# Kernel optimization log

Hardware: AMD Instinct MI355X
Metric: run time of the kernel (lower is better)

The kernel has to match this reference:

```python
import jax, jax.numpy as jnp
import numpy as np

N, E, DIN, HID, HEADS = 50000, 400000, 256, 64, 4
EPS_BN = 1e-5

def setup_inputs() -> dict:
    key = jax.random.key(0)
    ks = jax.random.split(key, 12)
    inp = {}
    inp['x'] = jax.random.normal(ks[0], (N, DIN), dtype=jnp.float32)
    inp['edge_index'] = jax.random.randint(ks[1], (2, E), 0, N, dtype=jnp.int64)
    s = 1.0 / np.sqrt(DIN)
    inp['W1'] = jax.random.uniform(ks[2], (DIN, HEADS * HID), jnp.float32, -s, s)
    inp['a_src1'] = jax.random.normal(ks[3], (HEADS, HID), dtype=jnp.float32) * 0.1
    inp['a_dst1'] = jax.random.normal(ks[4], (HEADS, HID), dtype=jnp.float32) * 0.1
    inp['b1'] = jnp.zeros((HEADS * HID,), jnp.float32)
    inp['bn1_w'] = jnp.ones((HEADS * HID,), jnp.float32)
    inp['bn1_b'] = jnp.zeros((HEADS * HID,), jnp.float32)
    inp['bn1_m'] = jnp.zeros((HEADS * HID,), jnp.float32)
    inp['bn1_v'] = jnp.ones((HEADS * HID,), jnp.float32)
    s2 = 1.0 / np.sqrt(HEADS * HID)
    inp['W2'] = jax.random.uniform(ks[5], (HEADS * HID, HID), jnp.float32, -s2, s2)
    inp['a_src2'] = jax.random.normal(ks[6], (1, HID), dtype=jnp.float32) * 0.1
    inp['a_dst2'] = jax.random.normal(ks[7], (1, HID), dtype=jnp.float32) * 0.1
    inp['b2'] = jnp.zeros((HID,), jnp.float32)
    inp['bn2_w'] = jnp.ones((HID,), jnp.float32)
    inp['bn2_b'] = jnp.zeros((HID,), jnp.float32)
    inp['bn2_m'] = jnp.zeros((HID,), jnp.float32)
    inp['bn2_v'] = jnp.ones((HID,), jnp.float32)
    sr = 1.0 / np.sqrt(HID)
    inp['Wr'] = jax.random.uniform(ks[8], (HID, 1), jnp.float32, -sr, sr)
    inp['br'] = jnp.zeros((1,), jnp.float32)
    inp['Wc'] = jax.random.uniform(ks[9], (HID, 1), jnp.float32, -sr, sr)
    inp['bc'] = jnp.zeros((1,), jnp.float32)
    return inp

def gat_layer(x, src, dst, W, a_src, a_dst, bias, concat):
    # x: [N, Fin] -> h: [N, H, D]
    H, D = a_src.shape
    h = (x @ W).reshape(-1, H, D)
    alpha_s = jnp.sum(h * a_src[None], axis=-1)  # [N, H]
    alpha_d = jnp.sum(h * a_dst[None], axis=-1)
    e = jax.nn.leaky_relu(alpha_s[src] + alpha_d[dst], 0.2)  # [Et, H]
    m = jax.ops.segment_max(e, dst, num_segments=N)
    m = jnp.where(jnp.isfinite(m), m, 0.0)
    ex = jnp.exp(e - m[dst])
    denom = jax.ops.segment_sum(ex, dst, num_segments=N)
    alpha = ex / (denom[dst] + 1e-16)  # segment softmax over incoming edges
    msg = h[src] * alpha[:, :, None]  # [Et, H, D]
    out = jax.ops.segment_sum(msg, dst, num_segments=N)  # [N, H, D]
    out = out.reshape(N, H * D) if concat else out.mean(axis=1)
    return out + bias

def batchnorm(x, w, b, mean, var):
    return (x - mean) * jax.lax.rsqrt(var + EPS_BN) * w + b

def reference(x, edge_index, W1, a_src1, a_dst1, b1, bn1_w, bn1_b, bn1_m, bn1_v,
              W2, a_src2, a_dst2, b2, bn2_w, bn2_b, bn2_m, bn2_v, Wr, br, Wc, bc):
    # add self loops (PyG GATConv default)
    loops = jnp.arange(N, dtype=edge_index.dtype)
    src = jnp.concatenate([edge_index[0], loops])
    dst = jnp.concatenate([edge_index[1], loops])
    h = gat_layer(x, src, dst, W1, a_src1, a_dst1, b1, concat=True)
    h = jax.nn.elu(batchnorm(h, bn1_w, bn1_b, bn1_m, bn1_v))
    h = gat_layer(h, src, dst, W2, a_src2, a_dst2, b2, concat=False)
    h = jax.nn.elu(batchnorm(h, bn2_w, bn2_b, bn2_m, bn2_v))
    reg = h @ Wr + br
    clf = jax.nn.sigmoid(h @ Wc + bc)
    return reg, clf
```

## Files before the change

kernel.cpp:

```cpp
#include <hip/hip_runtime.h>
#include <math.h>


typedef unsigned short ushort_t;
typedef unsigned char uchar_t;
typedef __attribute__((ext_vector_type(8))) unsigned short ushort8;
typedef __attribute__((ext_vector_type(4))) unsigned short ushort4v;
typedef __attribute__((ext_vector_type(8))) short short8;
typedef __attribute__((ext_vector_type(4))) float f32x4;
typedef __attribute__((ext_vector_type(2))) float f32x2;

#define EPS_BN 1e-5f

__device__ __forceinline__ ushort_t f2bf(float f) {
  unsigned u = __float_as_uint(f);
  unsigned r = u + 0x7fffu + ((u >> 16) & 1u);
  return (ushort_t)(r >> 16);
}
__device__ __forceinline__ float bf2f(ushort_t h) {
  return __uint_as_float((unsigned)h << 16);
}
__device__ __forceinline__ uchar_t f2fp8(float f) {
  return (uchar_t)(__builtin_amdgcn_cvt_pk_fp8_f32(f, f, 0, false) & 0xff);
}
__device__ __forceinline__ float leaky02(float x) { return x >= 0.f ? x : 0.2f * x; }
__device__ __forceinline__ float elu_fast(float x) {
  return x > 0.f ? x : __expf(x) - 1.f;
}
__device__ __forceinline__ float wave_sum(float v) {
#pragma unroll
  for (int o = 1; o < 64; o <<= 1) v += __shfl_xor(v, o, 64);
  return v;
}
__device__ __forceinline__ int wave_incl_scan(int v, int lane) {
#pragma unroll
  for (int off = 1; off < 64; off <<= 1) {
    int t = __shfl_up(v, off, 64);
    if (lane >= off) v += t;
  }
  return v;
}

__device__ __forceinline__ void gld_lds16(const ushort_t* g, ushort_t* l) {
  __builtin_amdgcn_global_load_lds(
      (const __attribute__((address_space(1))) unsigned int*)g,
      (__attribute__((address_space(3))) unsigned int*)l, 16, 0, 0);
}

__global__ __launch_bounds__(256) void hist_kernel(
    const int* __restrict__ dst, int* __restrict__ counts, int E,
    const float* __restrict__ x, ushort_t* __restrict__ xb, int n8) {
  int e = blockIdx.x * blockDim.x + threadIdx.x;
  if (e < E) atomicAdd(&counts[dst[e]], 1);
  const int gsz = gridDim.x * blockDim.x;
  for (int j = e; j < n8; j += gsz) {
    float4 f0 = *(const float4*)(x + (size_t)j * 8);
    float4 f1 = *(const float4*)(x + (size_t)j * 8 + 4);
    ushort8 u;
    u[0] = f2bf(f0.x); u[1] = f2bf(f0.y); u[2] = f2bf(f0.z); u[3] = f2bf(f0.w);
    u[4] = f2bf(f1.x); u[5] = f2bf(f1.y); u[6] = f2bf(f1.z); u[7] = f2bf(f1.w);
    *(ushort8*)(xb + (size_t)j * 8) = u;
  }
}

__global__ __launch_bounds__(256) void scan_chunks_kernel(
    const int* __restrict__ counts, int* __restrict__ offsets, int* __restrict__ partials,
    int N, int E, int* __restrict__ csr_src,
    const float* __restrict__ W1, const float* __restrict__ W2,
    ushort_t* __restrict__ W1t, ushort_t* __restrict__ W2t,
    const float* __restrict__ b1, const float* __restrict__ bn1w,
    const float* __restrict__ bn1b, const float* __restrict__ bn1m,
    const float* __restrict__ bn1v,
    const float* __restrict__ b2, const float* __restrict__ bn2w,
    const float* __restrict__ bn2b, const float* __restrict__ bn2m,
    const float* __restrict__ bn2v,
    float* __restrict__ S1, float* __restrict__ T1,
    float* __restrict__ S2, float* __restrict__ T2) {
  __shared__ int ws[4];
  const int tid = threadIdx.x, lane = tid & 63, wv = tid >> 6;
  const int i = blockIdx.x * 256 + tid;
  const int gsz = gridDim.x * 256;
  int v = (i < N) ? counts[i] : 0;
  int incl = wave_incl_scan(v, lane);
  if (lane == 63) ws[wv] = incl;
  __syncthreads();
  int wbase = 0;
  for (int k = 0; k < wv; ++k) wbase += ws[k];
  if (i < N) offsets[i] = wbase + incl - v;
  if (tid == 255) partials[blockIdx.x] = wbase + incl;

  for (int j = i; j < 256 * 256; j += gsz) {
    int k = j >> 8, n2 = j & 255;
    W1t[n2 * 256 + k] = f2bf(W1[j]);
  }
  for (int j = i; j < 256 * 64; j += gsz) {
    int k = j >> 6, n2 = j & 63;
    W2t[n2 * 256 + k] = f2bf(W2[j]);
  }
  if (i < 256) {
    float s = bn1w[i] * rsqrtf(bn1v[i] + EPS_BN);
    S1[i] = s;
    T1[i] = (b1[i] - bn1m[i]) * s + bn1b[i];
  } else if (i < 320) {
    int j = i - 256;
    float s = bn2w[j] * rsqrtf(bn2v[j] + EPS_BN);
    S2[j] = s;
    T2[j] = (b2[j] - bn2m[j]) * s + bn2b[j];
  } else if (i < 384) {
    csr_src[E + i - 320] = 0;
  }
}

__global__ __launch_bounds__(256) void scatter_kernel(
    const int* __restrict__ src, const int* __restrict__ dst,
    const int* __restrict__ offsets, const int* __restrict__ partials,
    int* __restrict__ cursor, int* __restrict__ csr_src,
    int* __restrict__ offs2, int E, int N, int nb) {
  __shared__ int pp[256];
  __shared__ int ws[4];
  __shared__ int tot;
  const int tid = threadIdx.x, lane = tid & 63, wv = tid >> 6;
  int v = (tid < nb) ? partials[tid] : 0;
  int incl = wave_incl_scan(v, lane);
  if (lane == 63) ws[wv] = incl;
  __syncthreads();
  int wbase = 0;
  for (int k = 0; k < wv; ++k) wbase += ws[k];
  pp[tid] = wbase + incl - v;
  if (tid == 255) tot = wbase + incl;
  __syncthreads();

  int idx = blockIdx.x * 256 + tid;
  if (idx < E) {
    int d = dst[idx];
    int p = atomicAdd(&cursor[d], 1);
    csr_src[offsets[d] + pp[d >> 8] + p] = src[idx];
  }
  if (idx <= N) {
    offs2[idx] = (idx < N) ? offsets[idx] + pp[idx >> 8] : tot;
  }
}

template <int WM, bool CASTA, int SWZ, int OUT8>
__global__ __launch_bounds__(WM * 64) void mfma_gemm_fused(
    const void* __restrict__ Ain, const ushort_t* __restrict__ Bt,
    void* __restrict__ Cout, const float* __restrict__ avs, const float* __restrict__ avd,
    float* __restrict__ as_out, float* __restrict__ ad_out, int M, int Nt, int K, int H) {
  constexpr int BM = WM * 32;
  constexpr int NB = 4 / WM;
  __shared__ ushort_t As[BM * 32];
  __shared__ ushort_t Bs[64 * 32];
  const int t = threadIdx.x;
  const int w = t >> 6, l = t & 63;
  int m0, n0;
  if (SWZ) {
    const int Mtile = (M + BM - 1) / BM;
    const int full = (Mtile & ~7) * 4;
    int id = blockIdx.x, r, c;
    if (id < full) {
      int grp = id >> 5, wd = id & 31;
      r = grp * 8 + (wd & 7);
      c = wd >> 3;
    } else {
      int tl = id - full;
      r = (Mtile & ~7) + (tl >> 2);
      c = tl & 3;
    }
    m0 = r * BM;
    n0 = c * 64;
  } else {
    m0 = blockIdx.y * BM;
    n0 = blockIdx.x * 64;
  }
  const int head = n0 >> 6;

  f32x4 zero4 = {0.f, 0.f, 0.f, 0.f};
  f32x4 acc[2][4];
#pragma unroll
  for (int i = 0; i < 2; ++i)
#pragma unroll
    for (int j = 0; j < 4; ++j) acc[i][j] = zero4;

  const int scol = (l & 3) * 8;
  const ushort_t* Bgb[NB];
  ushort_t* Bsl[NB];
#pragma unroll
  for (int b = 0; b < NB; ++b) {
    int r = (b * WM + w) * 16 + (l >> 2);
    Bgb[b] = Bt + (size_t)(n0 + r) * K + scol;
    Bsl[b] = &Bs[(b * WM + w) * 512];
  }
  const ushort_t* Aga[2];
  ushort_t* Asl[2];
  const float* Axg = nullptr;
  ushort_t* AsWc = nullptr;
  if (CASTA) {
    int ar = t >> 1, ac = (t & 1) * 16;
    Axg = (const float*)Ain + (size_t)min(m0 + ar, M - 1) * K + ac;
    AsWc = &As[ar * 32 + ac];
  } else {
#pragma unroll
    for (int a = 0; a < 2; ++a) {
      int r = (a * WM + w) * 16 + (l >> 2);
      int gr = min(m0 + r, M - 1);
      Aga[a] = (const ushort_t*)Ain + (size_t)gr * K + scol;
      Asl[a] = &As[(a * WM + w) * 512];
    }
  }

  for (int k0 = 0; k0 < K; k0 += 32) {
    if (CASTA) {
      float4 f0 = *(const float4*)(Axg + k0);
      float4 f1 = *(const float4*)(Axg + k0 + 4);
      float4 f2 = *(const float4*)(Axg + k0 + 8);
      float4 f3 = *(const float4*)(Axg + k0 + 12);
      __syncthreads();
#pragma unroll
      for (int b = 0; b < NB; ++b) gld_lds16(Bgb[b] + k0, Bsl[b]);
      ushort8 u0, u1;
      u0[0] = f2bf(f0.x); u0[1] = f2bf(f0.y); u0[2] = f2bf(f0.z); u0[3] = f2bf(f0.w);
      u0[4] = f2bf(f1.x); u0[5] = f2bf(f1.y); u0[6] = f2bf(f1.z); u0[7] = f2bf(f1.w);
      u1[0] = f2bf(f2.x); u1[1] = f2bf(f2.y); u1[2] = f2bf(f2.z); u1[3] = f2bf(f2.w);
      u1[4] = f2bf(f3.x); u1[5] = f2bf(f3.y); u1[6] = f2bf(f3.z); u1[7] = f2bf(f3.w);
      *(ushort8*)AsWc = u0;
      *(ushort8*)(AsWc + 8) = u1;
      __syncthreads();
    } else {
      __syncthreads();
#pragma unroll
      for (int a = 0; a < 2; ++a) gld_lds16(Aga[a] + k0, Asl[a]);
#pragma unroll
      for (int b = 0; b < NB; ++b) gld_lds16(Bgb[b] + k0, Bsl[b]);
      __syncthreads();
    }
    const int kq = (l >> 4) * 8;
    short8 af[2], bfr[4];
#pragma unroll
    for (int i = 0; i < 2; ++i)
      af[i] = *(const short8*)&As[(w * 32 + i * 16 + (l & 15)) * 32 + kq];
#pragma unroll
    for (int j = 0; j < 4; ++j)
      bfr[j] = *(const short8*)&Bs[(j * 16 + (l & 15)) * 32 + kq];
#pragma unroll
    for (int i = 0; i < 2; ++i)
#pragma unroll
      for (int j = 0; j < 4; ++j)
        acc[i][j] = __builtin_amdgcn_mfma_f32_16x16x32_bf16(af[i], bfr[j], acc[i][j], 0, 0, 0);
  }

  const int rbase = m0 + w * 32 + (l >> 4) * 4;
  const int cbase = n0 + (l & 15);
#pragma unroll
  for (int i = 0; i < 2; ++i)
#pragma unroll
    for (int j = 0; j < 4; ++j)
#pragma unroll
      for (int r = 0; r < 4; ++r) {
        int row = rbase + i * 16 + r;
        if (row < M) {
          if (OUT8)
            ((uchar_t*)Cout)[(size_t)row * Nt + cbase + j * 16] = f2fp8(acc[i][j][r]);
          else
            ((ushort_t*)Cout)[(size_t)row * Nt + cbase + j * 16] = f2bf(acc[i][j][r]);
        }
      }

  float asw[4], adw[4];
#pragma unroll
  for (int j = 0; j < 4; ++j) {
    asw[j] = avs[head * 64 + (l & 15) + j * 16];
    adw[j] = avd[head * 64 + (l & 15) + j * 16];
  }
#pragma unroll
  for (int i = 0; i < 2; ++i)
#pragma unroll
    for (int r = 0; r < 4; ++r) {
      float s_ = acc[i][0][r] * asw[0] + acc[i][1][r] * asw[1] +
                 acc[i][2][r] * asw[2] + acc[i][3][r] * asw[3];
      float d_ = acc[i][0][r] * adw[0] + acc[i][1][r] * adw[1] +
                 acc[i][2][r] * adw[2] + acc[i][3][r] * adw[3];
#pragma unroll
      for (int o = 1; o < 16; o <<= 1) {
        s_ += __shfl_xor(s_, o, 64);
        d_ += __shfl_xor(d_, o, 64);
      }
      if ((l & 15) == 0) {
        int row = rbase + i * 16 + r;
        if (row < M) {
          as_out[(size_t)row * H + head] = s_;
          ad_out[(size_t)row * H + head] = d_;
        }
      }
    }
}

__global__ __launch_bounds__(256) void agg1_kernel(
    const uchar_t* __restrict__ h1, const int* __restrict__ offsets,
    const int* __restrict__ csr, const float* __restrict__ as1,
    const float* __restrict__ ad1,
    const float* __restrict__ S1, const float* __restrict__ T1,
    ushort_t* __restrict__ out, int N) {
  __shared__ float ldsW[4][64][4];
  const int wv = threadIdx.x >> 6;
  int n = blockIdx.x * 4 + wv;
  int l = threadIdx.x & 63;
  if (n >= N) return;
  const int hh = l >> 4;
  int off = offsets[n], deg = offsets[n + 1] - off;
  const int* csrp = csr + off;
  const unsigned fb = (unsigned)l << 2;
  float4 adn = *(const float4*)&ad1[n * 4];
  float ad_h = (hh & 2) ? ((hh & 1) ? adn.w : adn.z) : ((hh & 1) ? adn.y : adn.x);

  f32x2 acc0 = {0.f, 0.f}, acc1 = {0.f, 0.f};
  float den = 0.f;

  for (int base = 0; base < deg; base += 64) {
    int cnt = min(64, deg - base);
    int s = 0;
    float4 w4 = make_float4(0.f, 0.f, 0.f, 0.f);
    if (l < cnt) {
      s = csrp[base + l];
      float4 a4 = *(const float4*)&as1[s * 4];
      w4.x = __expf(leaky02(a4.x + adn.x));
      w4.y = __expf(leaky02(a4.y + adn.y));
      w4.z = __expf(leaky02(a4.z + adn.z));
      w4.w = __expf(leaky02(a4.w + adn.w));
    }
    *(float4*)&ldsW[wv][l][0] = w4;
    for (int j = 0; j < cnt; j += 8) {
#pragma unroll
      for (int i = 0; i < 8; ++i) {
        int e = j + i;
        unsigned se = (unsigned)__builtin_amdgcn_readlane(s, e);
        float we = ldsW[wv][e][hh];
        unsigned q = *(const unsigned*)(h1 + (size_t)((se << 8) + fb));
        f32x2 lo = __builtin_amdgcn_cvt_pk_f32_fp8(q, false);
        f32x2 hi = __builtin_amdgcn_cvt_pk_f32_fp8(q, true);
        f32x2 w2 = {we, we};
        acc0 = lo * w2 + acc0;
        acc1 = hi * w2 + acc1;
        den += we;
      }
    }
  }

  float4 asn = *(const float4*)&as1[n * 4];
  float as_h = (hh & 2) ? ((hh & 1) ? asn.w : asn.z) : ((hh & 1) ? asn.y : asn.x);
  float ws = __expf(leaky02(as_h + ad_h));
  {
    unsigned q = *(const unsigned*)(h1 + (size_t)(((unsigned)n << 8) + fb));
    f32x2 lo = __builtin_amdgcn_cvt_pk_f32_fp8(q, false);
    f32x2 hi = __builtin_amdgcn_cvt_pk_f32_fp8(q, true);
    f32x2 w2 = {ws, ws};
    acc0 = lo * w2 + acc0;
    acc1 = hi * w2 + acc1;
  }
  float inv = 1.f / (den + ws + 1e-16f);

  const int c0 = l * 4;
  float4 Sv = *(const float4*)&S1[c0];
  float4 Tv = *(const float4*)&T1[c0];
  float o0 = fmaf(acc0.x, inv * Sv.x, Tv.x);
  float o1 = fmaf(acc0.y, inv * Sv.y, Tv.y);
  float o2 = fmaf(acc1.x, inv * Sv.z, Tv.z);
  float o3 = fmaf(acc1.y, inv * Sv.w, Tv.w);
  ushort4v o4;
  o4[0] = f2bf(elu_fast(o0));
  o4[1] = f2bf(elu_fast(o1));
  o4[2] = f2bf(elu_fast(o2));
  o4[3] = f2bf(elu_fast(o3));
  *(ushort4v*)&out[(size_t)n * 256 + c0] = o4;
}

__global__ __launch_bounds__(256) void agg2_kernel(
    const ushort_t* __restrict__ h2, const int* __restrict__ offsets,
    const int* __restrict__ csr, const float* __restrict__ as2,
    const float* __restrict__ ad2,
    const float* __restrict__ S2, const float* __restrict__ T2,
    const float* __restrict__ Wr, const float* __restrict__ br,
    const float* __restrict__ Wc, const float* __restrict__ bc,
    float* __restrict__ out_reg, float* __restrict__ out_clf, int N) {
  __shared__ float ldsW[4][64];
  __shared__ int ldsS[4][64];
  const int wv = threadIdx.x >> 6;
  int n = blockIdx.x * 4 + wv;
  int l = threadIdx.x & 63;
  if (n >= N) return;
  const int g = l >> 4, ll = l & 15;
  int off = offsets[n], deg = offsets[n + 1] - off;
  const int* csrp = csr + off;
  const size_t hoff = (size_t)ll * 4;
  float adn = ad2[n];

  float acc[4] = {0, 0, 0, 0};
  float ds = 0.f;

  for (int base = 0; base < deg; base += 64) {
    int cnt = min(64, deg - base);
    int s = 0;
    float wv_ = 0.f;
    if (l < cnt) {
      s = csrp[base + l];
      wv_ = __expf(leaky02(as2[s] + adn));
    }
    ldsS[wv][l] = s;
    ldsW[wv][l] = wv_;
    ds += wv_;
    for (int j = 0; j < cnt; j += 16) {
      int e0 = j + g, e1 = j + 4 + g, e2 = j + 8 + g, e3 = j + 12 + g;
      int s0 = ldsS[wv][e0], s1 = ldsS[wv][e1], s2 = ldsS[wv][e2], s3 = ldsS[wv][e3];
      float w0 = ldsW[wv][e0], w1 = ldsW[wv][e1], w2 = ldsW[wv][e2], w3 = ldsW[wv][e3];
      ushort4v r0 = *(const ushort4v*)&h2[(size_t)s0 * 64 + hoff];
      ushort4v r1 = *(const ushort4v*)&h2[(size_t)s1 * 64 + hoff];
      ushort4v r2 = *(const ushort4v*)&h2[(size_t)s2 * 64 + hoff];
      ushort4v r3 = *(const ushort4v*)&h2[(size_t)s3 * 64 + hoff];
#pragma unroll
      for (int k = 0; k < 4; ++k) acc[k] = fmaf(w0, bf2f(r0[k]), acc[k]);
#pragma unroll
      for (int k = 0; k < 4; ++k) acc[k] = fmaf(w1, bf2f(r1[k]), acc[k]);
#pragma unroll
      for (int k = 0; k < 4; ++k) acc[k] = fmaf(w2, bf2f(r2[k]), acc[k]);
#pragma unroll
      for (int k = 0; k < 4; ++k) acc[k] = fmaf(w3, bf2f(r3[k]), acc[k]);
    }
  }
#pragma unroll
  for (int k = 0; k < 4; ++k) {
    acc[k] += __shfl_xor(acc[k], 16, 64);
    acc[k] += __shfl_xor(acc[k], 32, 64);
  }
  float den = wave_sum(ds);
  float ws = __expf(leaky02(as2[n] + adn));
  ushort4v hn = *(const ushort4v*)&h2[(size_t)n * 64 + hoff];
#pragma unroll
  for (int k = 0; k < 4; ++k) acc[k] = fmaf(ws, bf2f(hn[k]), acc[k]);
  float inv = 1.f / (den + ws + 1e-16f);

  int c0 = ll * 4;
  float4 Sv = *(const float4*)&S2[c0];
  float4 Tv = *(const float4*)&T2[c0];
  float4 wr = *(const float4*)&Wr[c0];
  float4 wc = *(const float4*)&Wc[c0];
  float Sf[4] = {Sv.x, Sv.y, Sv.z, Sv.w};
  float Tf[4] = {Tv.x, Tv.y, Tv.z, Tv.w};
  float wrf[4] = {wr.x, wr.y, wr.z, wr.w};
  float wcf[4] = {wc.x, wc.y, wc.z, wc.w};
  float rs = 0.f, cs = 0.f;
#pragma unroll
  for (int q = 0; q < 4; ++q) {
    float o = fmaf(acc[q], inv * Sf[q], Tf[q]);
    o = elu_fast(o);
    rs = fmaf(o, wrf[q], rs);
    cs = fmaf(o, wcf[q], cs);
  }
#pragma unroll
  for (int o = 1; o < 16; o <<= 1) {
    rs += __shfl_xor(rs, o, 64);
    cs += __shfl_xor(cs, o, 64);
  }
  if (l == 0) {
    out_reg[n] = rs + br[0];
    float z = cs + bc[0];
    out_clf[n] = 1.f / (1.f + __expf(-z));
  }
}

extern "C" void kernel_launch(void* const* d_in, const int* in_sizes, int n_in,
                              void* d_out, int out_size, void* d_ws, size_t ws_size,
                              hipStream_t stream) {
  const float* x      = (const float*)d_in[0];
  const int*   ei     = (const int*)d_in[1];
  const float* W1     = (const float*)d_in[2];
  const float* a_src1 = (const float*)d_in[3];
  const float* a_dst1 = (const float*)d_in[4];
  const float* b1     = (const float*)d_in[5];
  const float* bn1w   = (const float*)d_in[6];
  const float* bn1b   = (const float*)d_in[7];
  const float* bn1m   = (const float*)d_in[8];
  const float* bn1v   = (const float*)d_in[9];
  const float* W2     = (const float*)d_in[10];
  const float* a_src2 = (const float*)d_in[11];
  const float* a_dst2 = (const float*)d_in[12];
  const float* b2     = (const float*)d_in[13];
  const float* bn2w   = (const float*)d_in[14];
  const float* bn2b   = (const float*)d_in[15];
  const float* bn2m   = (const float*)d_in[16];
  const float* bn2v   = (const float*)d_in[17];
  const float* Wr     = (const float*)d_in[18];
  const float* br     = (const float*)d_in[19];
  const float* Wc     = (const float*)d_in[20];
  const float* bc     = (const float*)d_in[21];

  const int N = in_sizes[0] / 256;
  const int E = in_sizes[1] / 2;
  const int* srcv = ei;
  const int* dstv = ei + E;

  char* w = (char*)d_ws;
  auto alloc = [&](size_t bytes) {
    char* p = w;
    w += (bytes + 255) & ~(size_t)255;
    return p;
  };
  const int nb = (N + 255) / 256;
  const size_t nbytes_rounded = ((size_t)N * 4 + 255) & ~(size_t)255;
  int* counts    = (int*)alloc((size_t)N * 4);
  int* cursor    = (int*)alloc((size_t)N * 4);
  int* offsets   = (int*)alloc((size_t)N * 4);
  int* offs2     = (int*)alloc((size_t)(N + 1) * 4);
  int* partials  = (int*)alloc((size_t)nb * 4);
  int* csr_src   = (int*)alloc((size_t)(E + 64) * 4);
  float* as1     = (float*)alloc((size_t)N * 4 * 4);
  float* ad1     = (float*)alloc((size_t)N * 4 * 4);
  float* as2     = (float*)alloc((size_t)N * 4);
  float* ad2     = (float*)alloc((size_t)N * 4);
  float* S1      = (float*)alloc(256 * 4);
  float* T1      = (float*)alloc(256 * 4);
  float* S2      = (float*)alloc(64 * 4);
  float* T2      = (float*)alloc(64 * 4);
  ushort_t* W1t  = (ushort_t*)alloc((size_t)256 * 256 * 2);
  ushort_t* W2t  = (ushort_t*)alloc((size_t)64 * 256 * 2);
  ushort_t* xb   = (ushort_t*)alloc((size_t)N * 256 * 2);
  uchar_t* h1b   = (uchar_t*)alloc((size_t)N * 256);
  ushort_t* h1a  = (ushort_t*)alloc((size_t)N * 256 * 2);
  ushort_t* h2b  = (ushort_t*)alloc((size_t)N * 64 * 2);

  float* out_reg = (float*)d_out;

  hipMemsetAsync(counts, 0, nbytes_rounded * 2, stream);
  hist_kernel<<<(E + 255) / 256, 256, 0, stream>>>(dstv, counts, E, x, xb, N * 256 / 8);
  scan_chunks_kernel<<<nb, 256, 0, stream>>>(counts, offsets, partials, N, E, csr_src,
                                             W1, W2, W1t, W2t,
                                             b1, bn1w, bn1b, bn1m, bn1v,
                                             b2, bn2w, bn2b, bn2m, bn2v,
                                             S1, T1, S2, T2);
  {
    int items = max(E, N + 1);
    scatter_kernel<<<(items + 255) / 256, 256, 0, stream>>>(srcv, dstv, offsets, partials,
                                                            cursor, csr_src, offs2, E, N, nb);
  }

  const int nwb = (N + 3) / 4;

  const int mtiles = (N + 127) / 128;
  mfma_gemm_fused<4, false, 1, 1><<<mtiles * 4, 256, 0, stream>>>(
      xb, W1t, h1b, a_src1, a_dst1, as1, ad1, N, 256, 256, 4);
  agg1_kernel<<<nwb, 256, 0, stream>>>(h1b, offs2, csr_src, as1, ad1, S1, T1, h1a, N);

  dim3 g2(1, (N + 63) / 64);
  mfma_gemm_fused<2, false, 0, 0><<<g2, 128, 0, stream>>>(h1a, W2t, h2b, a_src2, a_dst2,
                                                          as2, ad2, N, 64, 256, 1);
  agg2_kernel<<<nwb, 256, 0, stream>>>(h2b, offs2, csr_src, as2, ad2, S2, T2,
                                       Wr, br, Wc, bc, out_reg, out_reg + N, N);
}
```

Before: 260.7 us.

## Replace K-looped GEMM with full-K LDS-resident tiles and XCD-aware block remap

Both GEMMs now use one kernel that loads the whole 64x256 A tile and 64x256 B tile into LDS in a single pass, with an XOR swizzle against bank conflicts, and then runs the MFMA loop with no further barriers. This removes the per-K-step syncthreads and the load/compute serialization of the old 32-wide K loop. The first GEMM also remaps block IDs so neighbouring tiles land on the same XCD. The cost is 64 KB of LDS per block, which limits occupancy, and a 64-row M tile instead of 128 for layer 1.

```diff
diff --git a/kernel.cpp b/kernel.cpp
--- a/kernel.cpp
+++ b/kernel.cpp
@@ -141,157 +141,106 @@
   }
 }
 
-template <int WM, bool CASTA, int SWZ, int OUT8>
-__global__ __launch_bounds__(WM * 64) void mfma_gemm_fused(
-    const void* __restrict__ Ain, const ushort_t* __restrict__ Bt,
+template <int H, int OUT8, int SWZ>
+__global__ __launch_bounds__(256) void gemm_fullk(
+    const ushort_t* __restrict__ Ain, const ushort_t* __restrict__ Bt,
     void* __restrict__ Cout, const float* __restrict__ avs, const float* __restrict__ avd,
-    float* __restrict__ as_out, float* __restrict__ ad_out, int M, int Nt, int K, int H) {
-  constexpr int BM = WM * 32;
-  constexpr int NB = 4 / WM;
-  __shared__ ushort_t As[BM * 32];
-  __shared__ ushort_t Bs[64 * 32];
+    float* __restrict__ as_out, float* __restrict__ ad_out, int M) {
+  constexpr int NT = H * 64;
+  __shared__ ushort_t As[64 * 256];
+  __shared__ ushort_t Bs[64 * 256];
   const int t = threadIdx.x;
   const int w = t >> 6, l = t & 63;
-  int m0, n0;
+
+  int id = blockIdx.x;
   if (SWZ) {
-    const int Mtile = (M + BM - 1) / BM;
-    const int full = (Mtile & ~7) * 4;
-    int id = blockIdx.x, r, c;
-    if (id < full) {
-      int grp = id >> 5, wd = id & 31;
-      r = grp * 8 + (wd & 7);
-      c = wd >> 3;
-    } else {
-      int tl = id - full;
-      r = (Mtile & ~7) + (tl >> 2);
-      c = tl & 3;
-    }
-    m0 = r * BM;
-    n0 = c * 64;
-  } else {
-    m0 = blockIdx.y * BM;
-    n0 = blockIdx.x * 64;
-  }
-  const int head = n0 >> 6;
-
-  f32x4 zero4 = {0.f, 0.f, 0.f, 0.f};
-  f32x4 acc[2][4];
-#pragma unroll
-  for (int i = 0; i < 2; ++i)
-#pragma unroll
-    for (int j = 0; j < 4; ++j) acc[i][j] = zero4;
-
-  const int scol = (l & 3) * 8;
-  const ushort_t* Bgb[NB];
-  ushort_t* Bsl[NB];
-#pragma unroll
-  for (int b = 0; b < NB; ++b) {
-    int r = (b * WM + w) * 16 + (l >> 2);
-    Bgb[b] = Bt + (size_t)(n0 + r) * K + scol;
-    Bsl[b] = &Bs[(b * WM + w) * 512];
-  }
-  const ushort_t* Aga[2];
-  ushort_t* Asl[2];
-  const float* Axg = nullptr;
-  ushort_t* AsWc = nullptr;
-  if (CASTA) {
-    int ar = t >> 1, ac = (t & 1) * 16;
-    Axg = (const float*)Ain + (size_t)min(m0 + ar, M - 1) * K + ac;
-    AsWc = &As[ar * 32 + ac];
-  } else {
-#pragma unroll
-    for (int a = 0; a < 2; ++a) {
-      int r = (a * WM + w) * 16 + (l >> 2);
-      int gr = min(m0 + r, M - 1);
-      Aga[a] = (const ushort_t*)Ain + (size_t)gr * K + scol;
-      Asl[a] = &As[(a * WM + w) * 512];
-    }
-  }
-
-  for (int k0 = 0; k0 < K; k0 += 32) {
-    if (CASTA) {
-      float4 f0 = *(const float4*)(Axg + k0);
-      float4 f1 = *(const float4*)(Axg + k0 + 4);
-      float4 f2 = *(const float4*)(Axg + k0 + 8);
-      float4 f3 = *(const float4*)(Axg + k0 + 12);
-      __syncthreads();
-#pragma unroll
-      for (int b = 0; b < NB; ++b) gld_lds16(Bgb[b] + k0, Bsl[b]);
-      ushort8 u0, u1;
-      u0[0] = f2bf(f0.x); u0[1] = f2bf(f0.y); u0[2] = f2bf(f0.z); u0[3] = f2bf(f0.w);
-      u0[4] = f2bf(f1.x); u0[5] = f2bf(f1.y); u0[6] = f2bf(f1.z); u0[7] = f2bf(f1.w);
-      u1[0] = f2bf(f2.x); u1[1] = f2bf(f2.y); u1[2] = f2bf(f2.z); u1[3] = f2bf(f2.w);
-      u1[4] = f2bf(f3.x); u1[5] = f2bf(f3.y); u1[6] = f2bf(f3.z); u1[7] = f2bf(f3.w);
-      *(ushort8*)AsWc = u0;
-      *(ushort8*)(AsWc + 8) = u1;
-      __syncthreads();
-    } else {
-      __syncthreads();
-#pragma unroll
-      for (int a = 0; a < 2; ++a) gld_lds16(Aga[a] + k0, Asl[a]);
-#pragma unroll
-      for (int b = 0; b < NB; ++b) gld_lds16(Bgb[b] + k0, Bsl[b]);
-      __syncthreads();
-    }
-    const int kq = (l >> 4) * 8;
-    short8 af[2], bfr[4];
-#pragma unroll
-    for (int i = 0; i < 2; ++i)
-      af[i] = *(const short8*)&As[(w * 32 + i * 16 + (l & 15)) * 32 + kq];
-#pragma unroll
-    for (int j = 0; j < 4; ++j)
-      bfr[j] = *(const short8*)&Bs[(j * 16 + (l & 15)) * 32 + kq];
-#pragma unroll
-    for (int i = 0; i < 2; ++i)
-#pragma unroll
-      for (int j = 0; j < 4; ++j)
-        acc[i][j] = __builtin_amdgcn_mfma_f32_16x16x32_bf16(af[i], bfr[j], acc[i][j], 0, 0, 0);
-  }
-
-  const int rbase = m0 + w * 32 + (l >> 4) * 4;
-  const int cbase = n0 + (l & 15);
-#pragma unroll
-  for (int i = 0; i < 2; ++i)
-#pragma unroll
-    for (int j = 0; j < 4; ++j)
-#pragma unroll
-      for (int r = 0; r < 4; ++r) {
-        int row = rbase + i * 16 + r;
-        if (row < M) {
-          if (OUT8)
-            ((uchar_t*)Cout)[(size_t)row * Nt + cbase + j * 16] = f2fp8(acc[i][j][r]);
-          else
-            ((ushort_t*)Cout)[(size_t)row * Nt + cbase + j * 16] = f2bf(acc[i][j][r]);
-        }
+    const int nwg = gridDim.x;
+    const int q = nwg >> 3, rm = nwg & 7;
+    int xcd = id & 7, idx = id >> 3;
+    id = (xcd < rm ? xcd * (q + 1) : rm * (q + 1) + (xcd - rm) * q) + idx;
+  }
+  const int mt = (H == 1) ? id : (id >> 2);
+  const int head = (H == 1) ? 0 : (id & 3);
+  const int m0 = mt * 64;
+
+  {
+    const int slot = l & 7;
+#pragma unroll
+    for (int i = 0; i < 8; ++i) {
+      const int r = w * 64 + i * 8 + (l >> 3);
+      const int ir = r >> 2, kb = r & 3;
+      const int kc = (slot ^ (ir & 7)) << 3;
+      const int arow = min(m0 + ir, M - 1);
+      gld_lds16(Ain + (size_t)arow * 256 + kb * 64 + kc,
+                &As[w * 4096 + i * 512]);
+      const int brow = head * 64 + ir;
+      gld_lds16(Bt + (size_t)brow * 256 + kb * 64 + kc,
+                &Bs[w * 4096 + i * 512]);
+    }
+  }
+  __syncthreads();
+
+  f32x4 acc[4];
+#pragma unroll
+  for (int j = 0; j < 4; ++j) acc[j] = (f32x4){0.f, 0.f, 0.f, 0.f};
+
+  const int fr = l & 15;
+  const int kq = (l >> 4) << 3;
+  const int fx = (fr & 7) << 3;
+  const ushort_t* Ab = &As[(w * 16 + fr) << 8];
+  const ushort_t* Bb = &Bs[fr << 8];
+#pragma unroll
+  for (int k0 = 0; k0 < 256; k0 += 32) {
+    const int kabs = k0 + kq;
+    const int base = (kabs & ~63) + ((kabs & 63) ^ fx);
+    short8 af = *(const short8*)&Ab[base];
+#pragma unroll
+    for (int j = 0; j < 4; ++j) {
+      short8 bf8 = *(const short8*)&Bb[j * 4096 + base];
+      acc[j] = __builtin_amdgcn_mfma_f32_16x16x32_bf16(af, bf8, acc[j], 0, 0, 0);
+    }
+  }
+
+  const int rbase = m0 + w * 16 + (l >> 4) * 4;
+  const int cb = head * 64 + fr;
+#pragma unroll
+  for (int j = 0; j < 4; ++j)
+#pragma unroll
+    for (int r4 = 0; r4 < 4; ++r4) {
+      int row = rbase + r4;
+      if (row < M) {
+        if (OUT8)
+          ((uchar_t*)Cout)[(size_t)row * NT + cb + j * 16] = f2fp8(acc[j][r4]);
+        else
+          ((ushort_t*)Cout)[(size_t)row * NT + cb + j * 16] = f2bf(acc[j][r4]);
       }
+    }
 
   float asw[4], adw[4];
 #pragma unroll
   for (int j = 0; j < 4; ++j) {
-    asw[j] = avs[head * 64 + (l & 15) + j * 16];
-    adw[j] = avd[head * 64 + (l & 15) + j * 16];
-  }
-#pragma unroll
-  for (int i = 0; i < 2; ++i)
-#pragma unroll
-    for (int r = 0; r < 4; ++r) {
-      float s_ = acc[i][0][r] * asw[0] + acc[i][1][r] * asw[1] +
-                 acc[i][2][r] * asw[2] + acc[i][3][r] * asw[3];
-      float d_ = acc[i][0][r] * adw[0] + acc[i][1][r] * adw[1] +
-                 acc[i][2][r] * adw[2] + acc[i][3][r] * adw[3];
-#pragma unroll
-      for (int o = 1; o < 16; o <<= 1) {
-        s_ += __shfl_xor(s_, o, 64);
-        d_ += __shfl_xor(d_, o, 64);
+    asw[j] = avs[head * 64 + fr + j * 16];
+    adw[j] = avd[head * 64 + fr + j * 16];
+  }
+#pragma unroll
+  for (int r4 = 0; r4 < 4; ++r4) {
+    float s_ = acc[0][r4] * asw[0] + acc[1][r4] * asw[1] +
+               acc[2][r4] * asw[2] + acc[3][r4] * asw[3];
+    float d_ = acc[0][r4] * adw[0] + acc[1][r4] * adw[1] +
+               acc[2][r4] * adw[2] + acc[3][r4] * adw[3];
+#pragma unroll
+    for (int o = 1; o < 16; o <<= 1) {
+      s_ += __shfl_xor(s_, o, 64);
+      d_ += __shfl_xor(d_, o, 64);
+    }
+    if ((l & 15) == 0) {
+      int row = rbase + r4;
+      if (row < M) {
+        as_out[(size_t)row * H + head] = s_;
+        ad_out[(size_t)row * H + head] = d_;
       }
-      if ((l & 15) == 0) {
-        int row = rbase + i * 16 + r;
-        if (row < M) {
-          as_out[(size_t)row * H + head] = s_;
-          ad_out[(size_t)row * H + head] = d_;
-        }
-      }
-    }
+    }
+  }
 }
 
 __global__ __launch_bounds__(256) void agg1_kernel(
@@ -542,15 +491,14 @@
   }
 
   const int nwb = (N + 3) / 4;
-
-  const int mtiles = (N + 127) / 128;
-  mfma_gemm_fused<4, false, 1, 1><<<mtiles * 4, 256, 0, stream>>>(
-      xb, W1t, h1b, a_src1, a_dst1, as1, ad1, N, 256, 256, 4);
+  const int mtiles = (N + 63) / 64;
+
+  gemm_fullk<4, 1, 1><<<mtiles * 4, 256, 0, stream>>>(
+      xb, W1t, h1b, a_src1, a_dst1, as1, ad1, N);
   agg1_kernel<<<nwb, 256, 0, stream>>>(h1b, offs2, csr_src, as1, ad1, S1, T1, h1a, N);
 
-  dim3 g2(1, (N + 63) / 64);
-  mfma_gemm_fused<2, false, 0, 0><<<g2, 128, 0, stream>>>(h1a, W2t, h2b, a_src2, a_dst2,
-                                                          as2, ad2, N, 64, 256, 1);
+  gemm_fullk<1, 0, 0><<<mtiles, 256, 0, stream>>>(
+      h1a, W2t, h2b, a_src2, a_dst2, as2, ad2, N);
   agg2_kernel<<<nwb, 256, 0, stream>>>(h2b, offs2, csr_src, as2, ad2, S2, T2,
                                        Wr, br, Wc, bc, out_reg, out_reg + N, N);
 }
```

New measurement: 263.2 us. No clear change (+0.9%).
